# Performance work log

Measured on AMD Instinct MI355X. Metric: run time of the kernel, lower is better.

## Reference

```python
import jax, jax.numpy as jnp
import numpy as np

B, C, H, W = 2, 192, 128, 128
WS, OWS, HEADS = 16, 24, 6           # window, overlap window, heads
PAD = (OWS - WS) // 2
SCALE = (C // HEADS) ** -0.5
EPS = 1e-6


def _calc_rpi(ws, ows):
    co = np.stack(np.meshgrid(np.arange(ws), np.arange(ws), indexing='ij')).reshape(2, -1)
    ce = np.stack(np.meshgrid(np.arange(ows), np.arange(ows), indexing='ij')).reshape(2, -1)
    rel = (ce[:, None, :] - co[:, :, None]).transpose(1, 2, 0).astype(np.int64)  # (ws^2, ows^2, 2)
    rel[..., 0] += ws - ows + 1
    rel[..., 1] += ws - ows + 1
    rel[..., 0] *= ws + ows - 1
    idx = rel.sum(-1)
    # torch indexes the bias table with negative indices (python wraparound) -> explicit mod
    return np.mod(idx, (ws + ows - 1) ** 2)

RPI = jnp.asarray(_calc_rpi(WS, OWS))  # (WS*WS, OWS*OWS)


def _ln2d(x, g, b):  # LayerNorm2d over channel dim of (b,c,h,w)
    mu = jnp.mean(x, axis=1, keepdims=True)
    var = jnp.mean((x - mu) ** 2, axis=1, keepdims=True)
    return (x - mu) / jnp.sqrt(var + EPS) * g[None, :, None, None] + b[None, :, None, None]


def _conv1x1(x, w, b):  # x (b,c,h,w), w (o,c)
    return jnp.einsum('bchw,oc->bohw', x, w) + b[None, :, None, None]


def _window_partition(x, ws):  # (b,h,w,c) -> (b*nw, ws, ws, c)
    b, h, w, c = x.shape
    x = x.reshape(b, h // ws, ws, w // ws, ws, c).transpose(0, 1, 3, 2, 4, 5)
    return x.reshape(-1, ws, ws, c)


def _window_reverse(win, ws, h, w):  # (b*nw, ws, ws, c) -> (b,h,w,c)
    b = win.shape[0] // (h * w // ws // ws)
    x = win.reshape(b, h // ws, w // ws, ws, ws, -1).transpose(0, 1, 3, 2, 4, 5)
    return x.reshape(b, h, w, -1)


def _oca(x, qkv_w, qkv_b, rpb):  # overlapping-window cross attention; x (b,c,h,w), normalized
    b, c, h, w = x.shape
    qkv = jnp.einsum('bhwc,oc->bhwo', x.transpose(0, 2, 3, 1), qkv_w) + qkv_b
    qkv = qkv.reshape(b, h, w, 3, c).transpose(3, 0, 4, 1, 2)  # (3,b,c,h,w)
    q = qkv[0].transpose(0, 2, 3, 1)                            # (b,h,w,c)
    kv = jnp.concatenate([qkv[1], qkv[2]], axis=1)              # (b,2c,h,w)
    qw = _window_partition(q, WS).reshape(-1, WS * WS, c)
    # nn.Unfold(kernel=OWS, stride=WS, padding=PAD) replicated with padded gather
    p = jnp.pad(kv, ((0, 0), (0, 0), (PAD, PAD), (PAD, PAD)))
    nH, nW = h // WS, w // WS
    rows = (jnp.arange(nH) * WS)[:, None] + jnp.arange(OWS)[None, :]  # (nH, OWS)
    cols = (jnp.arange(nW) * WS)[:, None] + jnp.arange(OWS)[None, :]
    p = p[:, :, rows, :]            # (b,2c,nH,OWS,Wp)
    p = p[:, :, :, :, cols]         # (b,2c,nH,OWS,nW,OWS)
    p = p.reshape(b, 2, c, nH, OWS, nW, OWS).transpose(1, 0, 3, 5, 4, 6, 2)
    p = p.reshape(2, b * nH * nW, OWS * OWS, c)
    kwin, vwin = p[0], p[1]
    d = c // HEADS
    b_ = qw.shape[0]
    qh = qw.reshape(b_, WS * WS, HEADS, d).transpose(0, 2, 1, 3) * SCALE
    kh = kwin.reshape(b_, OWS * OWS, HEADS, d).transpose(0, 2, 1, 3)
    vh = vwin.reshape(b_, OWS * OWS, HEADS, d).transpose(0, 2, 1, 3)
    attn = jnp.einsum('bhqd,bhkd->bhqk', qh, kh)
    bias = rpb[RPI.reshape(-1)].reshape(WS * WS, OWS * OWS, HEADS).transpose(2, 0, 1)
    attn = jax.nn.softmax(attn + bias[None], axis=-1)
    out = jnp.einsum('bhqk,bhkd->bhqd', attn, vh).transpose(0, 2, 1, 3).reshape(b_, WS * WS, c)
    return _window_reverse(out.reshape(-1, WS, WS, c), WS, h, w)  # (b,h,w,c)


def setup_inputs() -> dict:
    key = jax.random.key(0)
    ks = jax.random.split(key, 16)
    s = 0.02
    return {
        'x_l': jax.random.normal(ks[0], (B, C, H, W), jnp.float32),
        'x_r': jax.random.normal(ks[1], (B, C, H, W), jnp.float32),
        'qkv_w': jax.random.normal(ks[2], (3 * C, C), jnp.float32) * s,
        'qkv_b': jnp.zeros((3 * C,), jnp.float32),
        'rpb_table': jax.random.normal(ks[3], ((WS + OWS - 1) ** 2, HEADS), jnp.float32) * s,
        'norm_l_g': jnp.ones((C,), jnp.float32),
        'norm_l_b': jnp.zeros((C,), jnp.float32),
        'norm_r_g': jnp.ones((C,), jnp.float32),
        'norm_r_b': jnp.zeros((C,), jnp.float32),
        'lp1_w': jax.random.normal(ks[4], (C, C), jnp.float32) * s,
        'lp1_b': jnp.zeros((C,), jnp.float32),
        'rp1_w': jax.random.normal(ks[5], (C, C), jnp.float32) * s,
        'rp1_b': jnp.zeros((C,), jnp.float32),
        'lp2_w': jax.random.normal(ks[6], (C, C), jnp.float32) * s,
        'lp2_b': jnp.zeros((C,), jnp.float32),
        'rp2_w': jax.random.normal(ks[7], (C, C), jnp.float32) * s,
        'rp2_b': jnp.zeros((C,), jnp.float32),
        'beta': jax.random.normal(ks[8], (1, C, 1, 1), jnp.float32) * s,
        'gamma': jax.random.normal(ks[9], (1, C, 1, 1), jnp.float32) * s,
    }


def reference(x_l, x_r, qkv_w, qkv_b, rpb_table, norm_l_g, norm_l_b, norm_r_g, norm_r_b,
              lp1_w, lp1_b, rp1_w, rp1_b, lp2_w, lp2_b, rp2_w, rp2_b, beta, gamma):
    nl = _ln2d(x_l, norm_l_g, norm_l_b)   # torch overwrites x_l with norm_l(x_l)
    nr = _ln2d(x_r, norm_r_g, norm_r_b)
    xl_ = _oca(nl, qkv_w, qkv_b, rpb_table)   # (b,h,w,c)
    xr_ = _oca(nr, qkv_w, qkv_b, rpb_table)
    Q_l = _conv1x1(_ln2d(xl_.transpose(0, 3, 2, 1), norm_l_g, norm_l_b), lp1_w, lp1_b).transpose(0, 2, 3, 1)  # (b,w,h,c)
    Q_r_T = _conv1x1(_ln2d(xr_.transpose(0, 3, 2, 1), norm_r_g, norm_r_b), rp1_w, rp1_b).transpose(0, 2, 1, 3)  # (b,w,c,h)
    V_l = _conv1x1(nl, lp2_w, lp2_b).transpose(0, 2, 3, 1)
    V_r = _conv1x1(nr, rp2_w, rp2_b).transpose(0, 2, 3, 1)
    att = jnp.matmul(Q_l, Q_r_T) * SCALE                       # (b,w,h,h) epipolar attention
    F_r2l = jnp.matmul(jax.nn.softmax(att, axis=-1), V_r)
    F_l2r = jnp.matmul(jax.nn.softmax(att.transpose(0, 1, 3, 2), axis=-1), V_l)
    out_l = nl + F_r2l.transpose(0, 3, 1, 2) * beta
    out_r = nr + F_l2r.transpose(0, 3, 1, 2) * gamma
    return (out_l, out_r)
```

## Files before the change

kernel.cpp:

```cpp
#include <hip/hip_runtime.h>
#include <stdint.h>

typedef short bf16x8 __attribute__((ext_vector_type(8)));
typedef float f32x4 __attribute__((ext_vector_type(4)));

__device__ inline float bf2f(uint16_t u){ uint32_t v = ((uint32_t)u)<<16; float f; __builtin_memcpy(&f,&v,4); return f; }
__device__ inline uint16_t f2bf(float f){ uint32_t u; __builtin_memcpy(&u,&f,4); u += 0x7fffu + ((u>>16)&1u); return (uint16_t)(u>>16); }

#define CCH   192
#define HH    128
#define WWD   128
#define HWSZ  16384
#define NPOS_SIDE 32768
#define NPOS  65536
#define NKT   576
#define SCALE_F 0.17677669529663687f

__global__ __launch_bounds__(256) void k_cvtw(const float* qkvw, const float* l1, const float* r1,
        const float* l2, const float* r2,
        uint16_t* wq, uint16_t* w1l, uint16_t* w1r, uint16_t* w2l, uint16_t* w2r){
    int which = blockIdx.y;
    int i = blockIdx.x*256 + threadIdx.x;
    const float* src; uint16_t* dst; int n;
    switch(which){
      case 0: src=qkvw; dst=wq;  n=576*192; break;
      case 1: src=l1;   dst=w1l; n=192*192; break;
      case 2: src=r1;   dst=w1r; n=192*192; break;
      case 3: src=l2;   dst=w2l; n=192*192; break;
      default:src=r2;   dst=w2r; n=192*192; break;
    }
    if(i<n) dst[i] = f2bf(src[i]);
}

__global__ __launch_bounds__(256) void k_bias(const float* rpb, uint32_t* biasP){
    int idx = blockIdx.x*256 + threadIdx.x;
    if(idx >= 6*256*18*16) return;
    int lr = idx & 15;
    int c  = (idx >> 4) % 18;
    int q  = (idx >> 4) / 18 % 256;
    int h  = idx / (16*18*256);
    int qi = q>>4, qj = q&15;
    uint32_t outw = 0;
    #pragma unroll
    for(int part=0; part<2; part++){
        int kt = c*32 + part*16 + lr;
        int ki = kt/24, kj = kt%24;
        int id = (ki - qi - 7)*39 + (kj - qj - 7);
        id %= 1521; if(id < 0) id += 1521;
        outw |= ((uint32_t)f2bf(rpb[id*6 + h])) << (16*part);
    }
    biasP[idx] = outw;
}

__global__ __launch_bounds__(256) void k_ln1(const float* xl, const float* xr,
        const float* gl, const float* bl, const float* gr, const float* br,
        uint16_t* nlr_bf){
    int pos = blockIdx.x*256 + threadIdx.x;
    int s   = pos >> 15;
    int loc = pos & 32767;
    const float* x = s ? xr : xl;
    const float* g = s ? gr : gl;
    const float* b = s ? br : bl;
    int bb = loc >> 14, hw = loc & 16383;
    const float* xp = x + (size_t)bb*CCH*HWSZ + hw;
    float sum=0.f, sq=0.f;
    for(int c=0;c<CCH;c++){ float v = xp[(size_t)c*HWSZ]; sum+=v; sq+=v*v; }
    float mean = sum*(1.f/192.f);
    float var  = sq*(1.f/192.f) - mean*mean;
    float rstd = rsqrtf(var + 1e-6f);
    uint16_t* obp = nlr_bf + (size_t)pos*CCH;
    for(int cb=0; cb<24; cb++){
        alignas(16) uint16_t tmp[8];
        #pragma unroll
        for(int k=0;k<8;k++){
            int c = cb*8+k;
            float y = (xp[(size_t)c*HWSZ]-mean)*rstd*g[c] + b[c];
            tmp[k] = f2bf(y);
        }
        *(uint4*)(obp + cb*8) = *(const uint4*)tmp;
    }
}

__global__ __launch_bounds__(256) void k_gemm(const uint16_t* __restrict__ A,
        const uint16_t* __restrict__ W, const float* __restrict__ bias,
        uint16_t* __restrict__ out, int K, int N){
    int tid = threadIdx.x;
    int w = tid >> 6, lane = tid & 63;
    int lr = lane & 15, lg = lane >> 4;
    int row0 = blockIdx.y*128 + w*16;
    int col0 = blockIdx.x*64;
    const uint16_t* Ap0 = A + (size_t)(row0 + lr)*K + lg*8;
    const uint16_t* Ap1 = Ap0 + (size_t)64*K;
    const uint16_t* Wp = W + (size_t)col0*K + lg*8;
    f32x4 acc[2][4] = {};
    int ksteps = K >> 5;
    for(int kk=0; kk<ksteps; kk++){
        bf16x8 a0 = *(const bf16x8*)(Ap0 + kk*32);
        bf16x8 a1 = *(const bf16x8*)(Ap1 + kk*32);
        #pragma unroll
        for(int nf=0; nf<4; nf++){
            bf16x8 bfr = *(const bf16x8*)(Wp + (size_t)(nf*16 + lr)*K + kk*32);
            acc[0][nf] = __builtin_amdgcn_mfma_f32_16x16x32_bf16(a0, bfr, acc[0][nf], 0,0,0);
            acc[1][nf] = __builtin_amdgcn_mfma_f32_16x16x32_bf16(a1, bfr, acc[1][nf], 0,0,0);
        }
    }
    #pragma unroll
    for(int nf=0; nf<4; nf++){
        int col = col0 + nf*16 + lr;
        float bv = bias[col];
        #pragma unroll
        for(int m=0; m<2; m++){
            #pragma unroll
            for(int r=0;r<4;r++){
                int row = row0 + m*64 + lg*4 + r;
                out[(size_t)row*N + col] = f2bf(acc[m][nf][r] + bv);
            }
        }
    }
}

#define KPAD 40
#define STG  192
#define VTP  200
__global__ __launch_bounds__(256) void k_attn(const uint16_t* __restrict__ qkv,
        const uint32_t* __restrict__ biasP, uint16_t* __restrict__ attout){
    __shared__ uint16_t Ks[STG*KPAD];
    __shared__ uint16_t Vt[32*VTP];
    __shared__ uint16_t Pw[4*64*KPAD];

    int bid = blockIdx.x;
    int s = bid / 768; int r1 = bid % 768;
    int b = r1 / 384;  int r2 = r1 % 384;
    int head = r2 / 64; int win = r2 % 64;
    int hb = win >> 3, wb = win & 7;
    int tid = threadIdx.x;
    int posbase = s*NPOS_SIDE + b*HWSZ;

    int wv = tid >> 6, lane = tid & 63;
    int lr = lane & 15, lg = lane >> 4;

    bf16x8 qA[4];
    #pragma unroll
    for(int f=0; f<4; f++){
        int t = wv*64 + f*16 + lr;
        int pos = posbase + (hb*16 + (t>>4))*WWD + (wb*16 + (t&15));
        qA[f] = *(const bf16x8*)(qkv + (size_t)pos*NKT + head*32 + lg*8);
    }

    f32x4 acc[4][2] = {};
    float psum[4][4];
    #pragma unroll
    for(int f=0;f<4;f++)
    #pragma unroll
    for(int r=0;r<4;r++) psum[f][r] = 0.f;

    const uint32_t* biasW = biasP + (size_t)head*256*18*16;
    uint16_t* myP = Pw + wv*64*KPAD;
    const uint16_t* kvbase = qkv + (size_t)posbase*NKT;

    for(int stg=0; stg<3; stg++){
        __syncthreads();
        for(int idx = tid; idx < STG*4; idx += 256){
            int ktl = idx >> 2, part = idx & 3;
            int ktg = stg*STG + ktl;
            int i = ktg/24, j = ktg%24;
            int h = hb*16 + i - 4, wv2 = wb*16 + j - 4;
            uint4 kd = {0,0,0,0}, vd = {0,0,0,0};
            if((unsigned)h < 128u && (unsigned)wv2 < 128u){
                const uint16_t* p = kvbase + (size_t)(h*WWD + wv2)*NKT + 192 + head*32 + part*8;
                kd = *(const uint4*)p;
                vd = *(const uint4*)(p + 192);
            }
            *(uint4*)(Ks + ktl*KPAD + part*8) = kd;
            const uint16_t* vs = (const uint16_t*)&vd;
            #pragma unroll
            for(int k2=0;k2<8;k2++) Vt[(part*8+k2)*VTP + ktl] = vs[k2];
        }
        __syncthreads();

        for(int kc=0; kc<6; kc++){
            int kt0 = kc*32;
            int cg  = stg*6 + kc;
            #pragma unroll
            for(int f=0; f<4; f++){
                f32x4 s0 = {}, s1 = {};
                bf16x8 b0 = *(const bf16x8*)(Ks + (kt0 + lr)*KPAD + lg*8);
                bf16x8 b1 = *(const bf16x8*)(Ks + (kt0 + 16 + lr)*KPAD + lg*8);
                s0 = __builtin_amdgcn_mfma_f32_16x16x32_bf16(qA[f], b0, s0, 0,0,0);
                s1 = __builtin_amdgcn_mfma_f32_16x16x32_bf16(qA[f], b1, s1, 0,0,0);
                int qrow = wv*64 + f*16 + lg*4;
                #pragma unroll
                for(int r=0;r<4;r++){
                    uint32_t bp = biasW[(size_t)(qrow+r)*18*16 + cg*16 + lr];
                    float v0 = s0[r]*SCALE_F + bf2f((uint16_t)(bp & 0xffff));
                    float v1 = s1[r]*SCALE_F + bf2f((uint16_t)(bp >> 16));
                    float e0 = __expf(v0), e1 = __expf(v1);
                    psum[f][r] += e0 + e1;
                    int prow = f*16 + lg*4 + r;
                    myP[prow*KPAD + lr]      = f2bf(e0);
                    myP[prow*KPAD + 16 + lr] = f2bf(e1);
                }
            }
            #pragma unroll
            for(int f=0; f<4; f++){
                bf16x8 pa = *(const bf16x8*)(myP + (f*16 + lr)*KPAD + lg*8);
                #pragma unroll
                for(int n=0;n<2;n++){
                    bf16x8 vb = *(const bf16x8*)(Vt + (n*16 + lr)*VTP + kt0 + lg*8);
                    acc[f][n] = __builtin_amdgcn_mfma_f32_16x16x32_bf16(pa, vb, acc[f][n], 0,0,0);
                }
            }
        }
    }

    #pragma unroll
    for(int f=0; f<4; f++){
        #pragma unroll
        for(int r=0;r<4;r++){
            float ssum = psum[f][r];
            ssum += __shfl_xor(ssum, 1);
            ssum += __shfl_xor(ssum, 2);
            ssum += __shfl_xor(ssum, 4);
            ssum += __shfl_xor(ssum, 8);
            psum[f][r] = 1.f / ssum;
        }
    }

    #pragma unroll
    for(int f=0; f<4; f++){
        #pragma unroll
        for(int r=0;r<4;r++){
            int t = wv*64 + f*16 + lg*4 + r;
            int pos = posbase + (hb*16 + (t>>4))*WWD + (wb*16 + (t&15));
            float inv = psum[f][r];
            #pragma unroll
            for(int n=0;n<2;n++){
                attout[(size_t)pos*CCH + head*32 + n*16 + lr] = f2bf(acc[f][n][r]*inv);
            }
        }
    }
}

__global__ __launch_bounds__(256) void k_ln2(const uint16_t* __restrict__ attout,
        const float* gl, const float* bl, const float* gr, const float* br,
        uint16_t* __restrict__ x2){
    int wv = threadIdx.x >> 6, lane = threadIdx.x & 63;
    int pos = blockIdx.x*4 + wv;
    int s = pos >> 15;
    const float* g = s ? gr : gl;
    const float* b = s ? br : bl;
    const uint16_t* ip = attout + (size_t)pos*CCH;
    float v[3]; float sum=0.f, sq=0.f;
    #pragma unroll
    for(int k=0;k<3;k++){ v[k] = bf2f(ip[lane + 64*k]); sum += v[k]; sq += v[k]*v[k]; }
    #pragma unroll
    for(int m=1;m<64;m<<=1){ sum += __shfl_xor(sum,m); sq += __shfl_xor(sq,m); }
    float mean = sum*(1.f/192.f);
    float var  = sq*(1.f/192.f) - mean*mean;
    float rstd = rsqrtf(var + 1e-6f);
    uint16_t* op = x2 + (size_t)pos*CCH;
    #pragma unroll
    for(int k=0;k<3;k++){
        int c = lane + 64*k;
        op[c] = f2bf((v[k]-mean)*rstd*g[c] + b[c]);
    }
}

__global__ __launch_bounds__(256) void k_cross1(const uint16_t* __restrict__ QL,
        const uint16_t* __restrict__ QR, uint16_t* __restrict__ Prow, uint16_t* __restrict__ PcolT){
    __shared__ float S[128*128];
    __shared__ float cred[2][128];
    __shared__ float colm[128];
    __shared__ float colinv[128];
    int bid = blockIdx.x; int b = bid >> 7, x = bid & 127;
    int tid = threadIdx.x;
    int wv = tid>>6, lane = tid&63, lr = lane&15, lg = lane>>4;
    const uint16_t* Abase = QL + (size_t)b*HWSZ*CCH;
    const uint16_t* Bbase = QR + (size_t)b*HWSZ*CCH;
    f32x4 acc[2][8] = {};
    for(int kk=0; kk<6; kk++){
        bf16x8 af[2];
        #pragma unroll
        for(int f=0;f<2;f++){
            int i = wv*32 + f*16 + lr;
            af[f] = *(const bf16x8*)(Abase + (size_t)(i*WWD + x)*CCH + kk*32 + lg*8);
        }
        #pragma unroll
        for(int nf=0; nf<8; nf++){
            int j = nf*16 + lr;
            bf16x8 bfr = *(const bf16x8*)(Bbase + (size_t)(j*WWD + x)*CCH + kk*32 + lg*8);
            #pragma unroll
            for(int f=0;f<2;f++)
                acc[f][nf] = __builtin_amdgcn_mfma_f32_16x16x32_bf16(af[f], bfr, acc[f][nf], 0,0,0);
        }
    }
    #pragma unroll
    for(int f=0;f<2;f++)
    #pragma unroll
    for(int nf=0;nf<8;nf++)
    #pragma unroll
    for(int r=0;r<4;r++){
        int i = wv*32 + f*16 + lg*4 + r; int j = nf*16 + lr;
        S[i*128 + j] = acc[f][nf][r]*SCALE_F;
    }
    __syncthreads();
    uint16_t* prb = Prow + (size_t)(b*128 + x)*128*128;
    for(int i = wv*32; i < wv*32+32; i++){
        float v0 = S[i*128 + lane], v1 = S[i*128 + 64 + lane];
        float m = fmaxf(v0,v1);
        #pragma unroll
        for(int k=1;k<64;k<<=1) m = fmaxf(m, __shfl_xor(m,k));
        float e0 = __expf(v0-m), e1 = __expf(v1-m);
        float ss = e0+e1;
        #pragma unroll
        for(int k=1;k<64;k<<=1) ss += __shfl_xor(ss,k);
        float inv = 1.f/ss;
        prb[i*128 + lane]      = f2bf(e0*inv);
        prb[i*128 + 64 + lane] = f2bf(e1*inv);
    }
    int j = tid & 127, half = tid >> 7;
    int i0 = half*64;
    float m = -1e30f;
    for(int i=i0; i<i0+64; i++) m = fmaxf(m, S[i*128 + j]);
    cred[half][j] = m;
    __syncthreads();
    if(tid < 128) colm[tid] = fmaxf(cred[0][tid], cred[1][tid]);
    __syncthreads();
    float mj = colm[j];
    float ssum = 0.f;
    for(int i=i0; i<i0+64; i++) ssum += __expf(S[i*128 + j] - mj);
    cred[half][j] = ssum;
    __syncthreads();
    if(tid < 128) colinv[tid] = 1.f/(cred[0][tid] + cred[1][tid]);
    __syncthreads();
    float cinv = colinv[j];
    uint16_t* pcb = PcolT + (size_t)(b*128 + x)*128*128;
    for(int i=i0; i<i0+64; i++) pcb[j*128 + i] = f2bf(__expf(S[i*128 + j] - mj)*cinv);
}

__global__ __launch_bounds__(256) void k_cross2(const uint16_t* __restrict__ Prow,
        const uint16_t* __restrict__ PcolT, const uint16_t* __restrict__ VR,
        const uint16_t* __restrict__ VL, const uint16_t* __restrict__ nlr_bf,
        const float* __restrict__ beta, const float* __restrict__ gamma, float* __restrict__ out){
    __shared__ uint16_t VT[192*136];
    int bid = blockIdx.x; int b = bid>>7, x = bid&127;
    int tid = threadIdx.x;
    int wv = tid>>6, lane = tid&63, lr = lane&15, lg = lane>>4;
    const uint16_t* vrs = VR + (size_t)(b*HWSZ + x*WWD)*CCH;
    const uint16_t* vls = VL + (size_t)(b*HWSZ + x*WWD)*CCH;
    const uint16_t* pr = Prow  + (size_t)(b*128+x)*128*128;
    const uint16_t* pc = PcolT + (size_t)(b*128+x)*128*128;

    for(int idx = tid; idx < 128*24; idx += 256){
        int j = idx / 24, cb = idx % 24;
        uint4 d = *(const uint4*)(vrs + j*CCH + cb*8);
        const uint16_t* dd = (const uint16_t*)&d;
        #pragma unroll
        for(int k=0;k<8;k++) VT[(cb*8+k)*136 + j] = dd[k];
    }
    __syncthreads();
    {
        f32x4 acc[2][12] = {};
        for(int kk=0; kk<4; kk++){
            bf16x8 af[2];
            #pragma unroll
            for(int f=0;f<2;f++){
                int i = wv*32 + f*16 + lr;
                af[f] = *(const bf16x8*)(pr + i*128 + kk*32 + lg*8);
            }
            #pragma unroll
            for(int nf=0; nf<12; nf++){
                bf16x8 bfr = *(const bf16x8*)(VT + (nf*16+lr)*136 + kk*32 + lg*8);
                #pragma unroll
                for(int f=0;f<2;f++)
                    acc[f][nf] = __builtin_amdgcn_mfma_f32_16x16x32_bf16(af[f], bfr, acc[f][nf], 0,0,0);
            }
        }
        #pragma unroll
        for(int nf=0; nf<12; nf++){
            int c = nf*16 + lr;
            float bv = beta[c];
            #pragma unroll
            for(int f=0; f<2; f++){
                int i0 = wv*32 + f*16 + lg*4;
                size_t o = ((size_t)(b*CCH + c)*128 + x)*128 + i0;
                const uint16_t* nb = nlr_bf + ((size_t)(b*HWSZ + x*WWD + i0))*CCH + c;
                float4 ov;
                ov.x = bf2f(nb[0*CCH]) + acc[f][nf][0]*bv;
                ov.y = bf2f(nb[1*CCH]) + acc[f][nf][1]*bv;
                ov.z = bf2f(nb[2*CCH]) + acc[f][nf][2]*bv;
                ov.w = bf2f(nb[3*CCH]) + acc[f][nf][3]*bv;
                *(float4*)(out + o) = ov;
            }
        }
    }
    __syncthreads();
    for(int idx = tid; idx < 128*24; idx += 256){
        int j = idx / 24, cb = idx % 24;
        uint4 d = *(const uint4*)(vls + j*CCH + cb*8);
        const uint16_t* dd = (const uint16_t*)&d;
        #pragma unroll
        for(int k=0;k<8;k++) VT[(cb*8+k)*136 + j] = dd[k];
    }
    __syncthreads();
    {
        f32x4 acc[2][12] = {};
        for(int kk=0; kk<4; kk++){
            bf16x8 af[2];
            #pragma unroll
            for(int f=0;f<2;f++){
                int j = wv*32 + f*16 + lr;
                af[f] = *(const bf16x8*)(pc + j*128 + kk*32 + lg*8);
            }
            #pragma unroll
            for(int nf=0; nf<12; nf++){
                bf16x8 bfr = *(const bf16x8*)(VT + (nf*16+lr)*136 + kk*32 + lg*8);
                #pragma unroll
                for(int f=0;f<2;f++)
                    acc[f][nf] = __builtin_amdgcn_mfma_f32_16x16x32_bf16(af[f], bfr, acc[f][nf], 0,0,0);
            }
        }
        float* outr = out + 6291456;
        #pragma unroll
        for(int nf=0; nf<12; nf++){
            int c = nf*16 + lr;
            float gv = gamma[c];
            #pragma unroll
            for(int f=0; f<2; f++){
                int j0 = wv*32 + f*16 + lg*4;
                size_t o = ((size_t)(b*CCH + c)*128 + x)*128 + j0;
                const uint16_t* nb = nlr_bf + ((size_t)(NPOS_SIDE + b*HWSZ + x*WWD + j0))*CCH + c;
                float4 ov;
                ov.x = bf2f(nb[0*CCH]) + acc[f][nf][0]*gv;
                ov.y = bf2f(nb[1*CCH]) + acc[f][nf][1]*gv;
                ov.z = bf2f(nb[2*CCH]) + acc[f][nf][2]*gv;
                ov.w = bf2f(nb[3*CCH]) + acc[f][nf][3]*gv;
                *(float4*)(outr + o) = ov;
            }
        }
    }
}

extern "C" void kernel_launch(void* const* d_in, const int* in_sizes, int n_in,
                              void* d_out, int out_size, void* d_ws, size_t ws_size,
                              hipStream_t stream){
    const float* x_l   = (const float*)d_in[0];
    const float* x_r   = (const float*)d_in[1];
    const float* qkv_w = (const float*)d_in[2];
    const float* qkv_b = (const float*)d_in[3];
    const float* rpb   = (const float*)d_in[4];
    const float* gl    = (const float*)d_in[5];
    const float* bl    = (const float*)d_in[6];
    const float* gr    = (const float*)d_in[7];
    const float* br    = (const float*)d_in[8];
    const float* lp1w  = (const float*)d_in[9];
    const float* lp1b  = (const float*)d_in[10];
    const float* rp1w  = (const float*)d_in[11];
    const float* rp1b  = (const float*)d_in[12];
    const float* lp2w  = (const float*)d_in[13];
    const float* lp2b  = (const float*)d_in[14];
    const float* rp2w  = (const float*)d_in[15];
    const float* rp2b  = (const float*)d_in[16];
    const float* beta  = (const float*)d_in[17];
    const float* gamma = (const float*)d_in[18];
    float* out = (float*)d_out;

    char* ws = (char*)d_ws;
    uint16_t* nlr_bf  = (uint16_t*)(ws + 0);
    uint16_t* qkv_bf  = (uint16_t*)(ws + 25165824);
    uint16_t* x2      = (uint16_t*)(ws + 25165824);
    uint16_t* QLb     = (uint16_t*)(ws + 50331648);
    uint16_t* QRb     = (uint16_t*)(ws + 62914560);
    uint16_t* Prow    = (uint16_t*)(ws + 75497472);
    uint16_t* PcolT   = (uint16_t*)(ws + 83886080);
    uint32_t* bias_p  = (uint32_t*)(ws + 100663296);
    uint16_t* attout  = (uint16_t*)(ws + 102432768);
    uint16_t* VLb     = (uint16_t*)(ws + 102432768);
    uint16_t* VRb     = (uint16_t*)(ws + 115015680);
    uint16_t* wq      = (uint16_t*)(ws + 127598592);
    uint16_t* w1l     = (uint16_t*)(ws + 127819776);
    uint16_t* w1r     = (uint16_t*)(ws + 127893504);
    uint16_t* w2l     = (uint16_t*)(ws + 127967232);
    uint16_t* w2r     = (uint16_t*)(ws + 128040960);

    k_cvtw<<<dim3(432,5), 256, 0, stream>>>(qkv_w, lp1w, rp1w, lp2w, rp2w, wq, w1l, w1r, w2l, w2r);
    k_bias<<<1728, 256, 0, stream>>>(rpb, bias_p);
    k_ln1<<<256, 256, 0, stream>>>(x_l, x_r, gl, bl, gr, br, nlr_bf);
    k_gemm<<<dim3(9, 512), 256, 0, stream>>>(nlr_bf, wq, qkv_b, qkv_bf, 192, 576);
    k_attn<<<1536, 256, 0, stream>>>(qkv_bf, bias_p, attout);
    k_ln2<<<16384, 256, 0, stream>>>(attout, gl, bl, gr, br, x2);
    k_gemm<<<dim3(3, 256), 256, 0, stream>>>(x2,                         w1l, lp1b, QLb, 192, 192);
    k_gemm<<<dim3(3, 256), 256, 0, stream>>>(x2 + (size_t)32768*192,     w1r, rp1b, QRb, 192, 192);
    k_gemm<<<dim3(3, 256), 256, 0, stream>>>(nlr_bf,                     w2l, lp2b, VLb, 192, 192);
    k_gemm<<<dim3(3, 256), 256, 0, stream>>>(nlr_bf + (size_t)32768*192, w2r, rp2b, VRb, 192, 192);
    k_cross1<<<256, 256, 0, stream>>>(QLb, QRb, Prow, PcolT);
    k_cross2<<<256, 256, 0, stream>>>(Prow, PcolT, VRb, VLb, nlr_bf, beta, gamma, out);
}
```

Measured before the change: 431.4 us.

## Compute transposed scores so softmax probs feed PV MFMA from registers

The attention kernel now computes S^T (K as A operand, Q as B) so each lane holds the probabilities in the layout needed as the A operand of the PV MFMA. This removes the shared-memory round trip for P and its LDS buffer. V is stored in LDS with a permuted key order to match, and the bias table is repacked so each lane loads its bias values as uint2. K/V fragment loads are hoisted out of the per-fragment loop, and the row-sum reduction becomes two cross-lane shuffles plus a broadcast. The risk is a mismatch in the permuted key ordering between P and V.

```diff
diff --git a/kernel.cpp b/kernel.cpp
--- a/kernel.cpp
+++ b/kernel.cpp
@@ -5,6 +5,7 @@
 typedef float f32x4 __attribute__((ext_vector_type(4)));
 
 __device__ inline float bf2f(uint16_t u){ uint32_t v = ((uint32_t)u)<<16; float f; __builtin_memcpy(&f,&v,4); return f; }
+__device__ inline float ubf(uint32_t u){ float f; __builtin_memcpy(&f,&u,4); return f; }
 __device__ inline uint16_t f2bf(float f){ uint32_t u; __builtin_memcpy(&u,&f,4); u += 0x7fffu + ((u>>16)&1u); return (uint16_t)(u>>16); }
 
 #define CCH   192
@@ -32,24 +33,26 @@
     if(i<n) dst[i] = f2bf(src[i]);
 }
 
-__global__ __launch_bounds__(256) void k_bias(const float* rpb, uint32_t* biasP){
-    int idx = blockIdx.x*256 + threadIdx.x;
-    if(idx >= 6*256*18*16) return;
-    int lr = idx & 15;
-    int c  = (idx >> 4) % 18;
-    int q  = (idx >> 4) / 18 % 256;
-    int h  = idx / (16*18*256);
-    int qi = q>>4, qj = q&15;
-    uint32_t outw = 0;
-    #pragma unroll
-    for(int part=0; part<2; part++){
-        int kt = c*32 + part*16 + lr;
+__global__ __launch_bounds__(256) void k_bias(const float* rpb, uint2* biasQ){
+    int e = blockIdx.x*256 + threadIdx.x;
+    if(e >= 6*256*18*8) return;
+    int k = e & 7;
+    int c = (e >> 3) % 18;
+    int q = ((e >> 3) / 18) % 256;
+    int h = e / (8*18*256);
+    int half = k >> 2, lg = k & 3;
+    int qi = q >> 4, qj = q & 15;
+    uint32_t w0 = 0, w1 = 0;
+    #pragma unroll
+    for(int r=0;r<4;r++){
+        int kt = c*32 + half*16 + lg*4 + r;
         int ki = kt/24, kj = kt%24;
         int id = (ki - qi - 7)*39 + (kj - qj - 7);
         id %= 1521; if(id < 0) id += 1521;
-        outw |= ((uint32_t)f2bf(rpb[id*6 + h])) << (16*part);
-    }
-    biasP[idx] = outw;
+        uint32_t bv = f2bf(rpb[id*6 + h]);
+        if(r < 2) w0 |= bv << (16*r); else w1 |= bv << (16*(r-2));
+    }
+    biasQ[e] = make_uint2(w0, w1);
 }
 
 __global__ __launch_bounds__(256) void k_ln1(const float* xl, const float* xr,
@@ -123,10 +126,9 @@
 #define STG  192
 #define VTP  200
 __global__ __launch_bounds__(256) void k_attn(const uint16_t* __restrict__ qkv,
-        const uint32_t* __restrict__ biasP, uint16_t* __restrict__ attout){
+        const uint2* __restrict__ biasQ, uint16_t* __restrict__ attout){
     __shared__ uint16_t Ks[STG*KPAD];
     __shared__ uint16_t Vt[32*VTP];
-    __shared__ uint16_t Pw[4*64*KPAD];
 
     int bid = blockIdx.x;
     int s = bid / 768; int r1 = bid % 768;
@@ -139,24 +141,19 @@
     int wv = tid >> 6, lane = tid & 63;
     int lr = lane & 15, lg = lane >> 4;
 
-    bf16x8 qA[4];
+    bf16x8 qB[4];
     #pragma unroll
     for(int f=0; f<4; f++){
         int t = wv*64 + f*16 + lr;
         int pos = posbase + (hb*16 + (t>>4))*WWD + (wb*16 + (t&15));
-        qA[f] = *(const bf16x8*)(qkv + (size_t)pos*NKT + head*32 + lg*8);
+        qB[f] = *(const bf16x8*)(qkv + (size_t)pos*NKT + head*32 + lg*8);
     }
 
     f32x4 acc[4][2] = {};
-    float psum[4][4];
-    #pragma unroll
-    for(int f=0;f<4;f++)
-    #pragma unroll
-    for(int r=0;r<4;r++) psum[f][r] = 0.f;
-
-    const uint32_t* biasW = biasP + (size_t)head*256*18*16;
-    uint16_t* myP = Pw + wv*64*KPAD;
+    float psum[4] = {0.f, 0.f, 0.f, 0.f};
+
     const uint16_t* kvbase = qkv + (size_t)posbase*NKT;
+    const uint2* biasH = biasQ + (size_t)head*256*18*8;
 
     for(int stg=0; stg<3; stg++){
         __syncthreads();
@@ -172,67 +169,62 @@
                 vd = *(const uint4*)(p + 192);
             }
             *(uint4*)(Ks + ktl*KPAD + part*8) = kd;
+            int t32 = ktl & 31;
+            int ktp = (ktl & ~31) + (((t32&12)<<1) + ((t32>>4)<<2) + (t32&3));
             const uint16_t* vs = (const uint16_t*)&vd;
             #pragma unroll
-            for(int k2=0;k2<8;k2++) Vt[(part*8+k2)*VTP + ktl] = vs[k2];
+            for(int k2=0;k2<8;k2++) Vt[(part*8+k2)*VTP + ktp] = vs[k2];
         }
         __syncthreads();
 
         for(int kc=0; kc<6; kc++){
             int kt0 = kc*32;
             int cg  = stg*6 + kc;
+            bf16x8 k0 = *(const bf16x8*)(Ks + (kt0 + lr)*KPAD + lg*8);
+            bf16x8 k1 = *(const bf16x8*)(Ks + (kt0 + 16 + lr)*KPAD + lg*8);
+            bf16x8 vb0 = *(const bf16x8*)(Vt + lr*VTP        + kt0 + lg*8);
+            bf16x8 vb1 = *(const bf16x8*)(Vt + (16+lr)*VTP   + kt0 + lg*8);
+
             #pragma unroll
             for(int f=0; f<4; f++){
-                f32x4 s0 = {}, s1 = {};
-                bf16x8 b0 = *(const bf16x8*)(Ks + (kt0 + lr)*KPAD + lg*8);
-                bf16x8 b1 = *(const bf16x8*)(Ks + (kt0 + 16 + lr)*KPAD + lg*8);
-                s0 = __builtin_amdgcn_mfma_f32_16x16x32_bf16(qA[f], b0, s0, 0,0,0);
-                s1 = __builtin_amdgcn_mfma_f32_16x16x32_bf16(qA[f], b1, s1, 0,0,0);
-                int qrow = wv*64 + f*16 + lg*4;
-                #pragma unroll
-                for(int r=0;r<4;r++){
-                    uint32_t bp = biasW[(size_t)(qrow+r)*18*16 + cg*16 + lr];
-                    float v0 = s0[r]*SCALE_F + bf2f((uint16_t)(bp & 0xffff));
-                    float v1 = s1[r]*SCALE_F + bf2f((uint16_t)(bp >> 16));
-                    float e0 = __expf(v0), e1 = __expf(v1);
-                    psum[f][r] += e0 + e1;
-                    int prow = f*16 + lg*4 + r;
-                    myP[prow*KPAD + lr]      = f2bf(e0);
-                    myP[prow*KPAD + 16 + lr] = f2bf(e1);
-                }
-            }
-            #pragma unroll
-            for(int f=0; f<4; f++){
-                bf16x8 pa = *(const bf16x8*)(myP + (f*16 + lr)*KPAD + lg*8);
-                #pragma unroll
-                for(int n=0;n<2;n++){
-                    bf16x8 vb = *(const bf16x8*)(Vt + (n*16 + lr)*VTP + kt0 + lg*8);
-                    acc[f][n] = __builtin_amdgcn_mfma_f32_16x16x32_bf16(pa, vb, acc[f][n], 0,0,0);
-                }
+                f32x4 z = {0.f,0.f,0.f,0.f};
+                f32x4 s0 = __builtin_amdgcn_mfma_f32_16x16x32_bf16(k0, qB[f], z, 0,0,0);
+                f32x4 s1 = __builtin_amdgcn_mfma_f32_16x16x32_bf16(k1, qB[f], z, 0,0,0);
+                int q = wv*64 + f*16 + lr;
+                const uint2* bq = biasH + ((size_t)q*18 + cg)*8;
+                uint2 bh0 = bq[lg];
+                uint2 bh1 = bq[4 + lg];
+                float e0 = __expf(__builtin_fmaf(s0[0], SCALE_F, ubf(bh0.x << 16)));
+                float e1 = __expf(__builtin_fmaf(s0[1], SCALE_F, ubf(bh0.x & 0xffff0000u)));
+                float e2 = __expf(__builtin_fmaf(s0[2], SCALE_F, ubf(bh0.y << 16)));
+                float e3 = __expf(__builtin_fmaf(s0[3], SCALE_F, ubf(bh0.y & 0xffff0000u)));
+                float e4 = __expf(__builtin_fmaf(s1[0], SCALE_F, ubf(bh1.x << 16)));
+                float e5 = __expf(__builtin_fmaf(s1[1], SCALE_F, ubf(bh1.x & 0xffff0000u)));
+                float e6 = __expf(__builtin_fmaf(s1[2], SCALE_F, ubf(bh1.y << 16)));
+                float e7 = __expf(__builtin_fmaf(s1[3], SCALE_F, ubf(bh1.y & 0xffff0000u)));
+                psum[f] += ((e0+e1)+(e2+e3)) + ((e4+e5)+(e6+e7));
+                bf16x8 pv;
+                pv[0] = (short)f2bf(e0); pv[1] = (short)f2bf(e1);
+                pv[2] = (short)f2bf(e2); pv[3] = (short)f2bf(e3);
+                pv[4] = (short)f2bf(e4); pv[5] = (short)f2bf(e5);
+                pv[6] = (short)f2bf(e6); pv[7] = (short)f2bf(e7);
+                acc[f][0] = __builtin_amdgcn_mfma_f32_16x16x32_bf16(pv, vb0, acc[f][0], 0,0,0);
+                acc[f][1] = __builtin_amdgcn_mfma_f32_16x16x32_bf16(pv, vb1, acc[f][1], 0,0,0);
             }
         }
     }
 
     #pragma unroll
     for(int f=0; f<4; f++){
+        float dsum = psum[f];
+        dsum += __shfl_xor(dsum, 16);
+        dsum += __shfl_xor(dsum, 32);
+        float invl = 1.f / dsum;
         #pragma unroll
         for(int r=0;r<4;r++){
-            float ssum = psum[f][r];
-            ssum += __shfl_xor(ssum, 1);
-            ssum += __shfl_xor(ssum, 2);
-            ssum += __shfl_xor(ssum, 4);
-            ssum += __shfl_xor(ssum, 8);
-            psum[f][r] = 1.f / ssum;
-        }
-    }
-
-    #pragma unroll
-    for(int f=0; f<4; f++){
-        #pragma unroll
-        for(int r=0;r<4;r++){
-            int t = wv*64 + f*16 + lg*4 + r;
-            int pos = posbase + (hb*16 + (t>>4))*WWD + (wb*16 + (t&15));
-            float inv = psum[f][r];
+            float inv = __shfl(invl, 4*lg + r);
+            int q = wv*64 + f*16 + 4*lg + r;
+            int pos = posbase + (hb*16 + (q>>4))*WWD + (wb*16 + (q&15));
             #pragma unroll
             for(int n=0;n<2;n++){
                 attout[(size_t)pos*CCH + head*32 + n*16 + lr] = f2bf(acc[f][n][r]*inv);
@@ -473,7 +465,7 @@
     uint16_t* QRb     = (uint16_t*)(ws + 62914560);
     uint16_t* Prow    = (uint16_t*)(ws + 75497472);
     uint16_t* PcolT   = (uint16_t*)(ws + 83886080);
-    uint32_t* bias_p  = (uint32_t*)(ws + 100663296);
+    uint2*    bias_q  = (uint2*)   (ws + 100663296);
     uint16_t* attout  = (uint16_t*)(ws + 102432768);
     uint16_t* VLb     = (uint16_t*)(ws + 102432768);
     uint16_t* VRb     = (uint16_t*)(ws + 115015680);
@@ -484,10 +476,10 @@
     uint16_t* w2r     = (uint16_t*)(ws + 128040960);
 
     k_cvtw<<<dim3(432,5), 256, 0, stream>>>(qkv_w, lp1w, rp1w, lp2w, rp2w, wq, w1l, w1r, w2l, w2r);
-    k_bias<<<1728, 256, 0, stream>>>(rpb, bias_p);
+    k_bias<<<864, 256, 0, stream>>>(rpb, bias_q);
     k_ln1<<<256, 256, 0, stream>>>(x_l, x_r, gl, bl, gr, br, nlr_bf);
     k_gemm<<<dim3(9, 512), 256, 0, stream>>>(nlr_bf, wq, qkv_b, qkv_bf, 192, 576);
-    k_attn<<<1536, 256, 0, stream>>>(qkv_bf, bias_p, attout);
+    k_attn<<<1536, 256, 0, stream>>>(qkv_bf, bias_q, attout);
     k_ln2<<<16384, 256, 0, stream>>>(attout, gl, bl, gr, br, x2);
     k_gemm<<<dim3(3, 256), 256, 0, stream>>>(x2,                         w1l, lp1b, QLb, 192, 192);
     k_gemm<<<dim3(3, 256), 256, 0, stream>>>(x2 + (size_t)32768*192,     w1r, rp1b, QRb, 192, 192);
```

New measurement: 397.1 us. -8.0%, faster.
